# Optimization experiments

Hardware: AMD Instinct MI355X
Metric: run time of the kernel (lower is better)

The kernel has to match this reference:

```python
import jax, jax.numpy as jnp
import numpy as np

NUM_HEADS = 12

def setup_inputs() -> dict:
    key = jax.random.key(0)
    k1, k2, k3, k4 = jax.random.split(key, 4)
    B, N, C = 64, 197, 768
    x = jax.random.normal(k1, (B, N, C), dtype=jnp.float32)
    w_qkv = jax.random.normal(k2, (3 * C, C), dtype=jnp.float32) * (C ** -0.5)
    w_proj = jax.random.normal(k3, (C, C), dtype=jnp.float32) * (C ** -0.5)
    b_proj = jax.random.normal(k4, (C,), dtype=jnp.float32) * 0.01
    return {"x": x, "w_qkv": w_qkv, "w_proj": w_proj, "b_proj": b_proj}

def reference(x, w_qkv, w_proj, b_proj):
    B, N, C = x.shape
    H = NUM_HEADS
    hd = C // H
    scale = hd ** -0.5
    # qkv linear (no bias): [B,N,3C] -> [3,B,H,N,hd]
    qkv = jnp.einsum('bnc,dc->bnd', x, w_qkv).reshape(B, N, 3, H, hd)
    qkv = jnp.transpose(qkv, (2, 0, 3, 1, 4))
    q, k, v = qkv[0], qkv[1], qkv[2]
    # full attention matrix [B,H,N,N] (materialized, matching the original)
    attn = jax.nn.softmax(jnp.einsum('bhnd,bhmd->bhnm', q, k) * scale, axis=-1)
    # CLS-token attention stats: mean over heads of attn row 0 (patch tokens) -> [B, N-1]
    global_attn = jnp.mean(attn[:, :, 0, 1:], axis=1)
    out = jnp.einsum('bhnm,bhmd->bhnd', attn, v)          # [B,H,N,hd]
    out = jnp.transpose(out, (0, 2, 1, 3)).reshape(B, N, C)
    out = jnp.einsum('bnc,dc->bnd', out, w_proj) + b_proj
    return out, global_attn
```

## Files before the change

kernel.cpp:

```cpp
#include <hip/hip_runtime.h>
#include <math.h>

#define B_   64
#define N_   197
#define C_   768
#define H_   12
#define HD_  64
#define BH_  (B_ * H_)
#define M_   (B_ * N_)

typedef _Float16 half8 __attribute__((ext_vector_type(8)));
typedef float    f32x4 __attribute__((ext_vector_type(4)));

#define XH_OFF   0u
#define WQH_OFF  19365888u
#define WPH_OFF  22904832u
#define QH_OFF   24084480u
#define KH_OFF   43450368u
#define VH_OFF   62816256u
#define OH_OFF   82182144u
#define P0_OFF   101548032u
#define WS_BYTES 102150144u

__device__ __forceinline__ half8 h8zero() {
    half8 z;
    #pragma unroll
    for (int i = 0; i < 8; ++i) z[i] = (_Float16)0;
    return z;
}

__device__ __forceinline__ void async16(const _Float16* g, _Float16* l) {
    __builtin_amdgcn_global_load_lds(
        (const __attribute__((address_space(1))) void*)g,
        (__attribute__((address_space(3))) void*)l,
        16, 0, 0);
}

__global__ void k_ws_too_small(float* out, float ws_bytes) { out[0] = -ws_bytes; }

__global__ __launch_bounds__(256) void k_cvt_all(const float* __restrict__ x,
                                                 const float* __restrict__ wq,
                                                 const float* __restrict__ wp,
                                                 _Float16* __restrict__ Xh,
                                                 _Float16* __restrict__ Wqh,
                                                 _Float16* __restrict__ Wph) {
    int i = blockIdx.x * blockDim.x + threadIdx.x;
    const float* src;
    _Float16*    dst;
    if (i < 1210368)      { src = x;  dst = Xh; }
    else if (i < 1431552) { src = wq; dst = Wqh; i -= 1210368; }
    else                  { src = wp; dst = Wph; i -= 1431552; }
    float4 f0 = *(const float4*)(src + (size_t)i * 8);
    float4 f1 = *(const float4*)(src + (size_t)i * 8 + 4);
    half8 h;
    h[0]=(_Float16)f0.x; h[1]=(_Float16)f0.y; h[2]=(_Float16)f0.z; h[3]=(_Float16)f0.w;
    h[4]=(_Float16)f1.x; h[5]=(_Float16)f1.y; h[6]=(_Float16)f1.z; h[7]=(_Float16)f1.w;
    *(half8*)(dst + (size_t)i * 8) = h;
}

__device__ __forceinline__ void mfma_nt_core_h(const _Float16* __restrict__ A,
                                               const _Float16* __restrict__ B,
                                               int M, int K, int m0, int n0,
                                               _Float16* As, _Float16* Bs,
                                               f32x4 (&acc)[4][4]) {
    const int tid  = threadIdx.x;
    const int wave = tid >> 6, lane = tid & 63;
    const int wr   = (wave >> 1) << 6;
    const int wc   = (wave & 1) << 6;
    const int ln   = lane & 15, kq = lane >> 4;

    const int row0 = tid >> 2;
    const int ch0  = (tid & 3) << 3;
    int ar0 = m0 + row0;        if (ar0 >= M) ar0 = 0;
    int ar1 = m0 + 64 + row0;   if (ar1 >= M) ar1 = 0;
    const _Float16* A0 = A + (size_t)ar0 * K + ch0;
    const _Float16* A1 = A + (size_t)ar1 * K + ch0;
    const _Float16* B0 = B + (size_t)(n0 + row0) * K + ch0;
    const _Float16* B1 = B + (size_t)(n0 + 64 + row0) * K + ch0;
    _Float16* AsD = As + (wave << 9);
    _Float16* BsD = Bs + (wave << 9);

    for (int k0 = 0; k0 < K; k0 += 32) {
        __syncthreads();
        async16(A0 + k0, AsD);
        async16(A1 + k0, AsD + 2048);
        async16(B0 + k0, BsD);
        async16(B1 + k0, BsD + 2048);
        __syncthreads();

        half8 af[4], bf[4];
        #pragma unroll
        for (int t = 0; t < 4; ++t) {
            af[t] = *(const half8*)&As[(wr + t * 16 + ln) * 32 + kq * 8];
            bf[t] = *(const half8*)&Bs[(wc + t * 16 + ln) * 32 + kq * 8];
        }
        #pragma unroll
        for (int i = 0; i < 4; ++i)
            #pragma unroll
            for (int j = 0; j < 4; ++j)
                acc[i][j] = __builtin_amdgcn_mfma_f32_16x16x32_f16(af[i], bf[j], acc[i][j], 0, 0, 0);
    }
}

__global__ __launch_bounds__(256) void k_qkv_mfma(const _Float16* __restrict__ Xh,
                                                  const _Float16* __restrict__ Wq,
                                                  _Float16* __restrict__ Qh,
                                                  _Float16* __restrict__ Kh,
                                                  _Float16* __restrict__ Vh) {
    __shared__ _Float16 As[128 * 32];
    __shared__ _Float16 Bs[128 * 32];
    const int m0 = blockIdx.y << 7;
    const int n0 = blockIdx.x << 7;
    f32x4 acc[4][4] = {};
    mfma_nt_core_h(Xh, Wq, M_, C_, m0, n0, As, Bs, acc);

    const int lane = threadIdx.x & 63;
    const int wave = threadIdx.x >> 6;
    const int wr = (wave >> 1) << 6, wc = (wave & 1) << 6;
    const int ln = lane & 15, kq = lane >> 4;
    #pragma unroll
    for (int mt = 0; mt < 4; ++mt) {
        #pragma unroll
        for (int i = 0; i < 4; ++i) {
            const int m = m0 + wr + mt * 16 + kq * 4 + i;
            if (m >= M_) continue;
            const int b = m / N_;
            const int n = m - b * N_;
            #pragma unroll
            for (int nt = 0; nt < 4; ++nt) {
                const int d  = n0 + wc + nt * 16 + ln;
                const int t3 = d / C_;
                const int rr = d - t3 * C_;
                const int h  = rr >> 6;
                const int e  = rr & 63;
                const size_t off = ((size_t)((b * H_ + h) * N_ + n)) * HD_ + e;
                const float v = acc[mt][nt][i];
                if      (t3 == 0) Qh[off] = (_Float16)(v * 0.125f);
                else if (t3 == 1) Kh[off] = (_Float16)v;
                else              Vh[off] = (_Float16)v;
            }
        }
    }
}

__global__ __launch_bounds__(256) void k_proj_mfma(const _Float16* __restrict__ Oh,
                                                   const _Float16* __restrict__ Wp,
                                                   const float* __restrict__ bias,
                                                   float* __restrict__ out) {
    __shared__ _Float16 As[128 * 32];
    __shared__ _Float16 Bs[128 * 32];
    const int m0 = blockIdx.y << 7;
    const int n0 = blockIdx.x << 7;
    f32x4 acc[4][4] = {};
    mfma_nt_core_h(Oh, Wp, M_, C_, m0, n0, As, Bs, acc);

    const int lane = threadIdx.x & 63;
    const int wave = threadIdx.x >> 6;
    const int wr = (wave >> 1) << 6, wc = (wave & 1) << 6;
    const int ln = lane & 15, kq = lane >> 4;
    float bv[4];
    #pragma unroll
    for (int nt = 0; nt < 4; ++nt) bv[nt] = bias[n0 + wc + nt * 16 + ln];
    #pragma unroll
    for (int mt = 0; mt < 4; ++mt) {
        #pragma unroll
        for (int i = 0; i < 4; ++i) {
            const int m = m0 + wr + mt * 16 + kq * 4 + i;
            if (m >= M_) continue;
            #pragma unroll
            for (int nt = 0; nt < 4; ++nt)
                out[(size_t)m * C_ + n0 + wc + nt * 16 + ln] = acc[mt][nt][i] + bv[nt];
        }
    }
}

__global__ __launch_bounds__(256) void k_attn(const _Float16* __restrict__ Qh,
                                              const _Float16* __restrict__ Kh,
                                              const _Float16* __restrict__ Vh,
                                              _Float16* __restrict__ Oh,
                                              float* __restrict__ P0) {
    __shared__ _Float16 lds[29824];
    _Float16* Ks = lds;
    _Float16* Pl = lds;
    _Float16* Vt = lds + 14976;

    const int bh = blockIdx.y, rt = blockIdx.x;
    const int b = bh / H_, h = bh - b * H_;
    const int tid = threadIdx.x, wave = tid >> 6, lane = tid & 63;
    const int ln = lane & 15, kq = lane >> 4;
    const size_t kvb = (size_t)bh * N_ * HD_;

    for (int idx = tid; idx < 208 * 8; idx += 256) {
        const int key = idx >> 3, c = (idx & 7) << 3;
        half8 v = (key < N_) ? *(const half8*)(Kh + kvb + (size_t)key * HD_ + c) : h8zero();
        *(half8*)&Ks[key * 72 + c] = v;
    }
    for (int idx = tid; idx < 197 * 8; idx += 256) {
        const int key = idx >> 3, c = (idx & 7) << 3;
        half8 v = *(const half8*)(Vh + kvb + (size_t)key * HD_ + c);
        #pragma unroll
        for (int j = 0; j < 8; ++j) Vt[(c + j) * 232 + key] = v[j];
    }
    for (int idx = tid; idx < 64 * 27; idx += 256) {
        const int d = idx / 27, k = 197 + (idx - d * 27);
        Vt[d * 232 + k] = (_Float16)0;
    }
    const int qrow = rt * 64 + wave * 16 + ln;
    const _Float16* Qp = Qh + kvb + (size_t)((qrow < N_) ? qrow : 0) * HD_ + kq * 8;
    half8 qf0 = *(const half8*)Qp;
    half8 qf1 = *(const half8*)(Qp + 32);
    __syncthreads();

    f32x4 acc[13] = {};
    #pragma unroll
    for (int c = 0; c < 13; ++c) {
        const _Float16* kp = &Ks[(c * 16 + ln) * 72 + kq * 8];
        half8 kf0 = *(const half8*)kp;
        half8 kf1 = *(const half8*)(kp + 32);
        acc[c] = __builtin_amdgcn_mfma_f32_16x16x32_f16(qf0, kf0, acc[c], 0, 0, 0);
        acc[c] = __builtin_amdgcn_mfma_f32_16x16x32_f16(qf1, kf1, acc[c], 0, 0, 0);
    }
    float inv4[4];
    #pragma unroll
    for (int r = 0; r < 4; ++r) {
        float m = -1e30f;
        #pragma unroll
        for (int c = 0; c < 13; ++c) {
            float x = ((c * 16 + ln) < N_) ? acc[c][r] : -1e30f;
            acc[c][r] = x;
            m = fmaxf(m, x);
        }
        m = fmaxf(m, __shfl_xor(m, 1)); m = fmaxf(m, __shfl_xor(m, 2));
        m = fmaxf(m, __shfl_xor(m, 4)); m = fmaxf(m, __shfl_xor(m, 8));
        float s = 0.f;
        #pragma unroll
        for (int c = 0; c < 13; ++c) { float e = __expf(acc[c][r] - m); acc[c][r] = e; s += e; }
        s += __shfl_xor(s, 1); s += __shfl_xor(s, 2);
        s += __shfl_xor(s, 4); s += __shfl_xor(s, 8);
        inv4[r] = 1.f / s;
    }
    __syncthreads();

    _Float16* Pw = Pl + wave * 16 * 232;
    #pragma unroll
    for (int c = 0; c < 13; ++c) {
        const int col = c * 16 + ln;
        #pragma unroll
        for (int r = 0; r < 4; ++r)
            Pw[(kq * 4 + r) * 232 + col] = (_Float16)(acc[c][r] * inv4[r]);
    }
    #pragma unroll
    for (int r = 0; r < 4; ++r) Pw[(kq * 4 + r) * 232 + 208 + ln] = (_Float16)0;

    if (rt == 0 && wave == 0 && kq == 0) {
        #pragma unroll
        for (int c = 0; c < 13; ++c) {
            const int col = c * 16 + ln;
            if (col >= 1 && col < N_) P0[(size_t)bh * 196 + col - 1] = acc[c][0] * inv4[0];
        }
    }
    __syncthreads();

    f32x4 o4[4] = {};
    for (int t = 0; t < 7; ++t) {
        half8 pf = *(const half8*)&Pw[ln * 232 + kq * 8 + 32 * t];
        #pragma unroll
        for (int n = 0; n < 4; ++n) {
            half8 vf = *(const half8*)&Vt[(n * 16 + ln) * 232 + kq * 8 + 32 * t];
            o4[n] = __builtin_amdgcn_mfma_f32_16x16x32_f16(pf, vf, o4[n], 0, 0, 0);
        }
    }
    const int g0 = rt * 64 + wave * 16 + kq * 4;
    #pragma unroll
    for (int r = 0; r < 4; ++r) {
        const int g = g0 + r;
        if (g >= N_) continue;
        _Float16* op = Oh + ((size_t)b * N_ + g) * C_ + h * HD_;
        #pragma unroll
        for (int n = 0; n < 4; ++n) op[n * 16 + ln] = (_Float16)o4[n][r];
    }
}

__global__ void k_gattn(const float* __restrict__ P0, float* __restrict__ out2) {
    const int idx = blockIdx.x * blockDim.x + threadIdx.x;
    const int b = idx / (N_ - 1), m = idx - b * (N_ - 1);
    float s = 0.f;
    #pragma unroll
    for (int h = 0; h < H_; ++h) s += P0[((size_t)(b * H_ + h)) * 196 + m];
    out2[idx] = s * (1.f / H_);
}

extern "C" void kernel_launch(void* const* d_in, const int* in_sizes, int n_in,
                              void* d_out, int out_size, void* d_ws, size_t ws_size,
                              hipStream_t stream) {
    const float* x      = (const float*)d_in[0];
    const float* w_qkv  = (const float*)d_in[1];
    const float* w_proj = (const float*)d_in[2];
    const float* b_proj = (const float*)d_in[3];
    float* out = (float*)d_out;
    char* ws   = (char*)d_ws;

    if (ws_size < (size_t)WS_BYTES) {
        k_ws_too_small<<<1, 1, 0, stream>>>(out, (float)ws_size);
        return;
    }

    _Float16* Xh  = (_Float16*)(ws + XH_OFF);
    _Float16* Wqh = (_Float16*)(ws + WQH_OFF);
    _Float16* Wph = (_Float16*)(ws + WPH_OFF);
    _Float16* Qh  = (_Float16*)(ws + QH_OFF);
    _Float16* Kh  = (_Float16*)(ws + KH_OFF);
    _Float16* Vh  = (_Float16*)(ws + VH_OFF);
    _Float16* Oh  = (_Float16*)(ws + OH_OFF);
    float*    P0  = (float*)   (ws + P0_OFF);

    k_cvt_all<<<5880, 256, 0, stream>>>(x, w_qkv, w_proj, Xh, Wqh, Wph);

    k_qkv_mfma <<<dim3(18, 99), 256, 0, stream>>>(Xh, Wqh, Qh, Kh, Vh);
    k_attn     <<<dim3(4, BH_), 256, 0, stream>>>(Qh, Kh, Vh, Oh, P0);
    k_gattn    <<<dim3(49),     256, 0, stream>>>(P0, out + (size_t)M_ * C_);
    k_proj_mfma<<<dim3(6, 99),  256, 0, stream>>>(Oh, Wph, b_proj, out);
}
```

Before: 261.1 us.

## Swizzle workgroups across XCDs, hoist QKV scatter math, add MFMA priority hints

Remaps the flat block index in the QKV GEMM, projection GEMM and attention kernels so that consecutive work tiles land on the same XCD, which should improve L2 reuse of shared weight and K/V tiles. The QKV epilogue now computes the destination base pointer and scale per column once, outside the row loop, instead of redoing the divisions and three-way branch for every element. In the attention kernel the MFMA loops are wrapped in s_setprio raises so waves issuing matrix work get scheduling priority. The swizzle assumes the grid sizes match the hardcoded tile counts.

```diff
diff --git a/kernel.cpp b/kernel.cpp
--- a/kernel.cpp
+++ b/kernel.cpp
@@ -34,6 +34,12 @@
         (const __attribute__((address_space(1))) void*)g,
         (__attribute__((address_space(3))) void*)l,
         16, 0, 0);
+}
+
+__device__ __forceinline__ int xcd_swz(int i, int nwg) {
+    const int q = nwg >> 3, r = nwg & 7;
+    const int xcd = i & 7, j = i >> 3;
+    return (xcd < r ? xcd * (q + 1) : r * (q + 1) + (xcd - r) * q) + j;
 }
 
 __global__ void k_ws_too_small(float* out, float ws_bytes) { out[0] = -ws_bytes; }
@@ -109,8 +115,9 @@
                                                   _Float16* __restrict__ Vh) {
     __shared__ _Float16 As[128 * 32];
     __shared__ _Float16 Bs[128 * 32];
-    const int m0 = blockIdx.y << 7;
-    const int n0 = blockIdx.x << 7;
+    const int work = xcd_swz(blockIdx.y * 18 + blockIdx.x, 18 * 99);
+    const int m0 = (work / 18) << 7;
+    const int n0 = (work % 18) << 7;
     f32x4 acc[4][4] = {};
     mfma_nt_core_h(Xh, Wq, M_, C_, m0, n0, As, Bs, acc);
 
@@ -118,6 +125,20 @@
     const int wave = threadIdx.x >> 6;
     const int wr = (wave >> 1) << 6, wc = (wave & 1) << 6;
     const int ln = lane & 15, kq = lane >> 4;
+
+    _Float16* basep[4];
+    float     scl[4];
+    #pragma unroll
+    for (int nt = 0; nt < 4; ++nt) {
+        const int d  = n0 + wc + nt * 16 + ln;
+        const int t3 = d / C_;
+        const int rr = d - t3 * C_;
+        const int h  = rr >> 6;
+        const int e  = rr & 63;
+        _Float16* t = (t3 == 0) ? Qh : (t3 == 1) ? Kh : Vh;
+        basep[nt] = t + (size_t)h * N_ * HD_ + e;
+        scl[nt]   = (t3 == 0) ? 0.125f : 1.f;
+    }
     #pragma unroll
     for (int mt = 0; mt < 4; ++mt) {
         #pragma unroll
@@ -126,19 +147,10 @@
             if (m >= M_) continue;
             const int b = m / N_;
             const int n = m - b * N_;
+            const size_t rowoff = ((size_t)b * H_ * N_ + n) * HD_;
             #pragma unroll
-            for (int nt = 0; nt < 4; ++nt) {
-                const int d  = n0 + wc + nt * 16 + ln;
-                const int t3 = d / C_;
-                const int rr = d - t3 * C_;
-                const int h  = rr >> 6;
-                const int e  = rr & 63;
-                const size_t off = ((size_t)((b * H_ + h) * N_ + n)) * HD_ + e;
-                const float v = acc[mt][nt][i];
-                if      (t3 == 0) Qh[off] = (_Float16)(v * 0.125f);
-                else if (t3 == 1) Kh[off] = (_Float16)v;
-                else              Vh[off] = (_Float16)v;
-            }
+            for (int nt = 0; nt < 4; ++nt)
+                basep[nt][rowoff] = (_Float16)(acc[mt][nt][i] * scl[nt]);
         }
     }
 }
@@ -149,8 +161,9 @@
                                                    float* __restrict__ out) {
     __shared__ _Float16 As[128 * 32];
     __shared__ _Float16 Bs[128 * 32];
-    const int m0 = blockIdx.y << 7;
-    const int n0 = blockIdx.x << 7;
+    const int work = xcd_swz(blockIdx.y * 6 + blockIdx.x, 6 * 99);
+    const int m0 = (work / 6) << 7;
+    const int n0 = (work % 6) << 7;
     f32x4 acc[4][4] = {};
     mfma_nt_core_h(Oh, Wp, M_, C_, m0, n0, As, Bs, acc);
 
@@ -184,7 +197,8 @@
     _Float16* Pl = lds;
     _Float16* Vt = lds + 14976;
 
-    const int bh = blockIdx.y, rt = blockIdx.x;
+    const int work = xcd_swz(blockIdx.y * 4 + blockIdx.x, 4 * BH_);
+    const int bh = work >> 2, rt = work & 3;
     const int b = bh / H_, h = bh - b * H_;
     const int tid = threadIdx.x, wave = tid >> 6, lane = tid & 63;
     const int ln = lane & 15, kq = lane >> 4;
@@ -212,6 +226,7 @@
     __syncthreads();
 
     f32x4 acc[13] = {};
+    __builtin_amdgcn_s_setprio(1);
     #pragma unroll
     for (int c = 0; c < 13; ++c) {
         const _Float16* kp = &Ks[(c * 16 + ln) * 72 + kq * 8];
@@ -220,6 +235,7 @@
         acc[c] = __builtin_amdgcn_mfma_f32_16x16x32_f16(qf0, kf0, acc[c], 0, 0, 0);
         acc[c] = __builtin_amdgcn_mfma_f32_16x16x32_f16(qf1, kf1, acc[c], 0, 0, 0);
     }
+    __builtin_amdgcn_s_setprio(0);
     float inv4[4];
     #pragma unroll
     for (int r = 0; r < 4; ++r) {
@@ -262,6 +278,7 @@
     __syncthreads();
 
     f32x4 o4[4] = {};
+    __builtin_amdgcn_s_setprio(1);
     for (int t = 0; t < 7; ++t) {
         half8 pf = *(const half8*)&Pw[ln * 232 + kq * 8 + 32 * t];
         #pragma unroll
@@ -270,6 +287,7 @@
             o4[n] = __builtin_amdgcn_mfma_f32_16x16x32_f16(pf, vf, o4[n], 0, 0, 0);
         }
     }
+    __builtin_amdgcn_s_setprio(0);
     const int g0 = rt * 64 + wave * 16 + kq * 4;
     #pragma unroll
     for (int r = 0; r < 4; ++r) {
```

Result: faster. 243.7 us (-6.7%).
